# Kernel optimization log

Measured on AMD Instinct MI355X. Metric: run time of the kernel, lower is better.

The kernel has to match this reference:

```python
import jax, jax.numpy as jnp
import numpy as np

FP8_E4M3_MAX = 448.0  # matches the 448.0 constant in the torch module


def setup_inputs() -> dict:
    key = jax.random.key(0)
    kx, kw, kb = jax.random.split(key, 3)
    B, S, D_IN, D_OUT = 4, 2048, 4096, 4096
    x = jax.random.normal(kx, (B, S, D_IN), dtype=jnp.float32)
    # Simulate the __init__-time FP8 quantization of the linear weight.
    w = jax.random.normal(kw, (D_OUT, D_IN), dtype=jnp.float32) * 0.02
    amax = jnp.max(jnp.abs(w))
    weight_scale = FP8_E4M3_MAX / (amax + 1e-12)
    weight_fp8 = (w * weight_scale).astype(jnp.float8_e4m3fn)  # stored FP8 buffer
    weight_inv_scale = (1.0 / weight_scale).astype(jnp.float32)
    bias = jax.random.normal(kb, (D_OUT,), dtype=jnp.float32) * 0.02
    return {"x": x, "weight_fp8": weight_fp8,
            "weight_inv_scale": weight_inv_scale, "bias": bias}


def reference(x, weight_fp8, weight_inv_scale, bias):
    # forward: dequantize FP8 weight to compute dtype, scale, then dense linear
    w = weight_fp8.astype(x.dtype) * weight_inv_scale.astype(x.dtype)  # [D_OUT, D_IN]
    # F.linear(x, w, bias) == x @ w.T + bias
    return jnp.einsum('bsd,od->bso', x, w) + bias.astype(x.dtype)
```

## Files before the change

kernel.cpp:

```cpp
#include <hip/hip_runtime.h>
#include <hip/hip_bf16.h>
#include <stdint.h>
#include <stddef.h>

typedef __bf16 bf16x8 __attribute__((ext_vector_type(8)));
typedef float  f32x4  __attribute__((ext_vector_type(4)));

__device__ __forceinline__ float fp8e4m3_to_f32(uint32_t b) {
    uint32_t e = (b >> 3) & 15u, m = b & 7u;
    float mag;
    if (e == 0)
        mag = (float)m * (1.0f / 512.0f);
    else
        mag = __uint_as_float(((e + 120u) << 23) | (m << 20));
    return (b & 0x80u) ? -mag : mag;
}

__device__ __forceinline__ unsigned short f32_to_bf16_bits(float f) {
    uint32_t x = __float_as_uint(f);
    uint32_t r = x + 0x7fffu + ((x >> 16) & 1u);
    return (unsigned short)(r >> 16);
}

__device__ __forceinline__ void gload_lds16(const void* g, void* l) {
    __builtin_amdgcn_global_load_lds(
        (const __attribute__((address_space(1))) uint32_t*)g,
        (__attribute__((address_space(3))) uint32_t*)l,
        16, 0, 0);
}

__global__ void detect_kernel(const uint32_t* __restrict__ w,
                              uint32_t* __restrict__ flag) {
    __shared__ int sF, sB;
    if (threadIdx.x == 0) { sF = 1; sB = 1; }
    __syncthreads();
    int f32ok = 1, bf16ok = 1;
    #pragma unroll
    for (int i = 0; i < 16; ++i) {
        uint32_t u = w[threadIdx.x * 16 + i];
        if (u & 0x000FFFFFu) f32ok = 0;
        if (u & 0x000F000Fu) bf16ok = 0;
    }
    if (!f32ok)  atomicExch(&sF, 0);
    if (!bf16ok) atomicExch(&sB, 0);
    __syncthreads();
    if (threadIdx.x == 0)
        *flag = sF ? 0u : (sB ? 1u : 2u);
}

__global__ void cvt_x_kernel(const float* __restrict__ x,
                             unsigned short* __restrict__ out, size_t n8) {
    size_t stride = (size_t)gridDim.x * blockDim.x;
    for (size_t i = (size_t)blockIdx.x * blockDim.x + threadIdx.x; i < n8; i += stride) {
        const float4* p = (const float4*)(x + i * 8);
        float4 a = p[0], b = p[1];
        union { uint4 v; unsigned short s[8]; } o;
        o.s[0] = f32_to_bf16_bits(a.x); o.s[1] = f32_to_bf16_bits(a.y);
        o.s[2] = f32_to_bf16_bits(a.z); o.s[3] = f32_to_bf16_bits(a.w);
        o.s[4] = f32_to_bf16_bits(b.x); o.s[5] = f32_to_bf16_bits(b.y);
        o.s[6] = f32_to_bf16_bits(b.z); o.s[7] = f32_to_bf16_bits(b.w);
        *(uint4*)(out + i * 8) = o.v;
    }
}

__global__ void prep_w_kernel(const void* __restrict__ wsrc,
                              const uint32_t* __restrict__ flag,
                              unsigned short* __restrict__ out, size_t n8) {
    const uint32_t mode = *flag;
    size_t stride = (size_t)gridDim.x * blockDim.x;
    for (size_t i = (size_t)blockIdx.x * blockDim.x + threadIdx.x; i < n8; i += stride) {
        union { uint4 v; unsigned short s[8]; } o;
        if (mode == 0) {
            const float4* p = (const float4*)((const float*)wsrc + i * 8);
            float4 a = p[0], b = p[1];
            o.s[0] = f32_to_bf16_bits(a.x); o.s[1] = f32_to_bf16_bits(a.y);
            o.s[2] = f32_to_bf16_bits(a.z); o.s[3] = f32_to_bf16_bits(a.w);
            o.s[4] = f32_to_bf16_bits(b.x); o.s[5] = f32_to_bf16_bits(b.y);
            o.s[6] = f32_to_bf16_bits(b.z); o.s[7] = f32_to_bf16_bits(b.w);
        } else if (mode == 1) {
            o.v = *(const uint4*)((const unsigned short*)wsrc + i * 8);
        } else {
            union { uint2 v; uint8_t b[8]; } u;
            u.v = *(const uint2*)((const uint8_t*)wsrc + i * 8);
            #pragma unroll
            for (int j = 0; j < 8; ++j)
                o.s[j] = f32_to_bf16_bits(fp8e4m3_to_f32(u.b[j]));
        }
        *(uint4*)(out + i * 8) = o.v;
    }
}


#define GBM 256
#define GBN 256
#define GBK 64

#define LDA_(qm) do {                                                          \
    _Pragma("unroll") for (int m = 0; m < 4; ++m) {                            \
        Af[m][0] = *(const bf16x8*)(a0 + ((qm)*8192 + m*2048));                \
        Af[m][1] = *(const bf16x8*)(a1 + ((qm)*8192 + m*2048));                \
    }                                                                          \
} while (0)

#define LDB_(qn, Bf) do {                                                      \
    _Pragma("unroll") for (int n = 0; n < 2; ++n) {                            \
        Bf[n][0] = *(const bf16x8*)(b0 + ((qn)*4096 + n*2048));                \
        Bf[n][1] = *(const bf16x8*)(b1 + ((qn)*4096 + n*2048));                \
    }                                                                          \
} while (0)

#define MFMA_(qm, qn, Bf) do {                                                 \
    _Pragma("unroll") for (int m = 0; m < 4; ++m)                              \
    _Pragma("unroll") for (int n = 0; n < 2; ++n)                              \
    _Pragma("unroll") for (int ks = 0; ks < 2; ++ks)                           \
        acc[(qm)*4+m][(qn)*2+n] = __builtin_amdgcn_mfma_f32_16x16x32_bf16(     \
            Af[m][ks], Bf[n][ks], acc[(qm)*4+m][(qn)*2+n], 0, 0, 0);           \
} while (0)

#define STAGE_(gsrc, koff, ldst) do {                                          \
    const uint8_t* _p = (gsrc) + (koff);                                       \
    _Pragma("unroll") for (int j = 0; j < 4; ++j)                              \
        gload_lds16(_p + (size_t)j * 64 * KB2, (ldst) + (sdst + j*8192));      \
} while (0)

__global__ __launch_bounds__(512, 2)
void gemm256_fr(const unsigned short* __restrict__ A,
                const unsigned short* __restrict__ Bw,
                const float* __restrict__ invp,
                const float* __restrict__ bias,
                float* __restrict__ C, int M, int N, int K) {
    __shared__ unsigned short lds[2][2][GBM * GBK];
    char* ldsb = (char*)&lds[0][0][0];

    const size_t KB2 = (size_t)K * 2;
    const int KT = K / GBK;

    const int nwg = gridDim.x;
    const int b   = blockIdx.x;
    const int wg  = (b & 7) * (nwg >> 3) + (b >> 3);
    const int MT  = M / GBM;
    const int tm  = wg % MT;
    const int tn  = wg / MT;

    const int t     = threadIdx.x;
    const int lane  = t & 63;
    const int wid   = t >> 6;
    const int wm    = wid >> 2;
    const int wn    = wid & 3;
    const int laneQ = lane & 15;
    const int laneH = lane >> 4;
    const int xorv  = (laneQ & 7) << 4;
    const int lrow  = lane >> 3;
    const int lcb   = (lane & 7) ^ lrow;

    const int col0  = (0   + laneH * 16) ^ xorv;
    const int col1  = (64  + laneH * 16) ^ xorv;
    const int aoff0 = wm * 16384 + laneQ * 128 + col0;
    const int aoff1 = wm * 16384 + laneQ * 128 + col1;
    const int boff0 = wn * 8192  + laneQ * 128 + col0;
    const int boff1 = wn * 8192  + laneQ * 128 + col1;
    const int sdst  = wid * 1024 + lane * 16;

    const uint8_t* gA = (const uint8_t*)A +
        ((size_t)tm * GBM + wid * 8 + lrow) * KB2 + (size_t)lcb * 16;
    const uint8_t* gB = (const uint8_t*)Bw +
        ((size_t)tn * GBN + wid * 8 + lrow) * KB2 + (size_t)lcb * 16;

    f32x4 acc[8][4] = {};
    bf16x8 Af[4][2], B0[2][2], B1[2][2];

    STAGE_(gB, (size_t)0,   ldsb + 32768);
    STAGE_(gA, (size_t)0,   ldsb);
    STAGE_(gB, (size_t)128, ldsb + 65536 + 32768);
    STAGE_(gA, (size_t)128, ldsb + 65536);
    asm volatile("s_waitcnt vmcnt(8)" ::: "memory");
    __builtin_amdgcn_s_barrier();

    for (int kt = 0; kt < KT; ++kt) {
        const int coff = (kt & 1) << 16;
        const char* ldsA = ldsb + coff;
        const char* ldsB = ldsb + coff + 32768;
        const char* a0 = ldsA + aoff0;
        const char* a1 = ldsA + aoff1;
        const char* b0 = ldsB + boff0;
        const char* b1 = ldsB + boff1;
        char* ldsAw = (char*)ldsA;
        char* ldsBw = (char*)ldsB;
        const bool more = (kt + 2) < KT;
        const size_t kb2 = (size_t)(kt + 2) * 128;

        LDA_(0);
        LDB_(0, B0);
        __builtin_amdgcn_s_setprio(1);
        MFMA_(0, 0, B0);
        __builtin_amdgcn_s_setprio(0);
        LDB_(1, B1);
        __builtin_amdgcn_s_setprio(1);
        MFMA_(0, 1, B1);
        __builtin_amdgcn_s_setprio(0);
        LDA_(1);
        asm volatile("s_waitcnt lgkmcnt(0)" ::: "memory");
        __builtin_amdgcn_s_barrier();

        if (more) {
            STAGE_(gB, kb2, ldsBw);
            STAGE_(gA, kb2, ldsAw);
        }
        __builtin_amdgcn_s_setprio(1);
        MFMA_(1, 1, B1);
        MFMA_(1, 0, B0);
        __builtin_amdgcn_s_setprio(0);
        if (more) asm volatile("s_waitcnt vmcnt(8)" ::: "memory");
        else      asm volatile("s_waitcnt vmcnt(0)" ::: "memory");
        __builtin_amdgcn_s_barrier();
    }

    const float inv = *invp;
    float bv[4];
    #pragma unroll
    for (int n = 0; n < 4; ++n)
        bv[n] = bias[tn * GBN + wn * 64 + n * 16 + laneQ];

    #pragma unroll
    for (int m = 0; m < 8; ++m) {
        int rowb = tm * GBM + wm * 128 + m * 16 + laneH * 4;
        #pragma unroll
        for (int j = 0; j < 4; ++j) {
            float* cp = C + (size_t)(rowb + j) * N + tn * GBN + wn * 64;
            #pragma unroll
            for (int n = 0; n < 4; ++n)
                cp[n * 16 + laneQ] = acc[m][n][j] * inv + bv[n];
        }
    }
}

__global__ void naive_kernel(const float* __restrict__ x,
                             const void* __restrict__ wsrc,
                             const uint32_t* flag,
                             const float* __restrict__ invp,
                             const float* __restrict__ bias,
                             float* __restrict__ out, int M, int N, int K) {
    const uint32_t mode = flag ? *flag : 0u;
    size_t idx = (size_t)blockIdx.x * blockDim.x + threadIdx.x;
    if (idx >= (size_t)M * N) return;
    int m = (int)(idx / N), n = (int)(idx % N);
    const float* xr = x + (size_t)m * K;
    float s = 0.f;
    if (mode == 0) {
        const float* wr = (const float*)wsrc + (size_t)n * K;
        for (int k = 0; k < K; ++k) s += xr[k] * wr[k];
    } else if (mode == 1) {
        const unsigned short* wr = (const unsigned short*)wsrc + (size_t)n * K;
        for (int k = 0; k < K; ++k)
            s += xr[k] * __uint_as_float(((uint32_t)wr[k]) << 16);
    } else {
        const uint8_t* wr = (const uint8_t*)wsrc + (size_t)n * K;
        for (int k = 0; k < K; ++k) s += xr[k] * fp8e4m3_to_f32(wr[k]);
    }
    out[idx] = s * (*invp) + bias[n];
}

extern "C" void kernel_launch(void* const* d_in, const int* in_sizes, int n_in,
                              void* d_out, int out_size, void* d_ws, size_t ws_size,
                              hipStream_t stream) {
    const float*    x    = (const float*)d_in[0];
    const void*     wsrc = d_in[1];
    const float*    inv  = (const float*)d_in[2];
    const float*    bias = (const float*)d_in[3];
    float*          out  = (float*)d_out;

    const int K = in_sizes[1] / in_sizes[3];
    const int N = in_sizes[3];
    const int M = in_sizes[0] / K;

    const size_t needA = (size_t)M * K * sizeof(unsigned short);
    const size_t needB = (size_t)N * K * sizeof(unsigned short);

    const bool shape_ok = (M % GBM) == 0 && (N % GBN) == 0 && (K % GBK) == 0 &&
                          (K / GBK) >= 2 &&
                          (((M / GBM) * (N / GBN)) % 8) == 0;

    if (ws_size < needA + needB + 256 || !shape_ok) {
        size_t total = (size_t)M * N;
        uint32_t* flag = (ws_size >= 256) ? (uint32_t*)d_ws : nullptr;
        if (flag) detect_kernel<<<1, 256, 0, stream>>>((const uint32_t*)wsrc, flag);
        naive_kernel<<<(unsigned)((total + 255) / 256), 256, 0, stream>>>(
            x, wsrc, flag, inv, bias, out, M, N, K);
        return;
    }

    uint32_t*       flag = (uint32_t*)d_ws;
    unsigned short* Abf  = (unsigned short*)((char*)d_ws + 256);
    unsigned short* Wbf  = (unsigned short*)((char*)d_ws + 256 + needA);

    detect_kernel<<<1, 256, 0, stream>>>((const uint32_t*)wsrc, flag);
    cvt_x_kernel<<<2048, 256, 0, stream>>>(x, Abf, (size_t)M * K / 8);
    prep_w_kernel<<<2048, 256, 0, stream>>>(wsrc, flag, Wbf, (size_t)N * K / 8);

    dim3 grid((M / GBM) * (N / GBN));
    gemm256_fr<<<grid, 512, 0, stream>>>(Abf, Wbf, inv, bias, out, M, N, K);
}
```

Baseline: 297.4 us.

## Prefetch next tile's B fragments from LDS across the barrier

Restructures the main loop so the first B fragment set for the next k-tile is loaded from the other LDS buffer right after the end-of-iteration barrier, before the last MFMA group runs. The MFMA groups are reordered so that MFMA(1,0) runs before the barrier and MFMA(1,1) runs after it. This is meant to hide LDS read latency behind MFMA work and put more compute between the global-stage issue and the wait. In exchange it keeps an extra fragment set live across iterations, which raises register pressure, and it moves the global staging issue later relative to compute.

After: 301.5 us. Within noise of the previous version (+1.4%).

```diff
diff --git a/kernel.cpp b/kernel.cpp
--- a/kernel.cpp
+++ b/kernel.cpp
@@ -97,24 +97,26 @@
 
 #define LDA_(qm) do {                                                          \
     _Pragma("unroll") for (int m = 0; m < 4; ++m) {                            \
-        Af[m][0] = *(const bf16x8*)(a0 + ((qm)*8192 + m*2048));                \
-        Af[m][1] = *(const bf16x8*)(a1 + ((qm)*8192 + m*2048));                \
+        AF[m][0] = *(const bf16x8*)(ldsA + aoff0 + ((qm)*8192 + m*2048));      \
+        AF[m][1] = *(const bf16x8*)(ldsA + aoff1 + ((qm)*8192 + m*2048));      \
     }                                                                          \
 } while (0)
 
-#define LDB_(qn, Bf) do {                                                      \
+#define LDB_(base, qn, Bf) do {                                                \
     _Pragma("unroll") for (int n = 0; n < 2; ++n) {                            \
-        Bf[n][0] = *(const bf16x8*)(b0 + ((qn)*4096 + n*2048));                \
-        Bf[n][1] = *(const bf16x8*)(b1 + ((qn)*4096 + n*2048));                \
+        Bf[n][0] = *(const bf16x8*)((base) + boff0 + ((qn)*4096 + n*2048));    \
+        Bf[n][1] = *(const bf16x8*)((base) + boff1 + ((qn)*4096 + n*2048));    \
     }                                                                          \
 } while (0)
 
 #define MFMA_(qm, qn, Bf) do {                                                 \
+    __builtin_amdgcn_s_setprio(1);                                             \
     _Pragma("unroll") for (int m = 0; m < 4; ++m)                              \
     _Pragma("unroll") for (int n = 0; n < 2; ++n)                              \
     _Pragma("unroll") for (int ks = 0; ks < 2; ++ks)                           \
         acc[(qm)*4+m][(qn)*2+n] = __builtin_amdgcn_mfma_f32_16x16x32_bf16(     \
-            Af[m][ks], Bf[n][ks], acc[(qm)*4+m][(qn)*2+n], 0, 0, 0);           \
+            AF[m][ks], Bf[n][ks], acc[(qm)*4+m][(qn)*2+n], 0, 0, 0);           \
+    __builtin_amdgcn_s_setprio(0);                                             \
 } while (0)
 
 #define STAGE_(gsrc, koff, ldst) do {                                          \
@@ -124,7 +126,7 @@
 } while (0)
 
 __global__ __launch_bounds__(512, 2)
-void gemm256_fr(const unsigned short* __restrict__ A,
+void gemm256_pf(const unsigned short* __restrict__ A,
                 const unsigned short* __restrict__ Bw,
                 const float* __restrict__ invp,
                 const float* __restrict__ bias,
@@ -167,7 +169,7 @@
         ((size_t)tn * GBN + wid * 8 + lrow) * KB2 + (size_t)lcb * 16;
 
     f32x4 acc[8][4] = {};
-    bf16x8 Af[4][2], B0[2][2], B1[2][2];
+    bf16x8 AF[4][2], BX[2][2], BY[2][2];
 
     STAGE_(gB, (size_t)0,   ldsb + 32768);
     STAGE_(gA, (size_t)0,   ldsb);
@@ -175,30 +177,25 @@
     STAGE_(gA, (size_t)128, ldsb + 65536);
     asm volatile("s_waitcnt vmcnt(8)" ::: "memory");
     __builtin_amdgcn_s_barrier();
+    LDB_(ldsb + 32768, 0, BX);
 
     for (int kt = 0; kt < KT; ++kt) {
         const int coff = (kt & 1) << 16;
-        const char* ldsA = ldsb + coff;
-        const char* ldsB = ldsb + coff + 32768;
-        const char* a0 = ldsA + aoff0;
-        const char* a1 = ldsA + aoff1;
-        const char* b0 = ldsB + boff0;
-        const char* b1 = ldsB + boff1;
+        const char* ldsA  = ldsb + coff;
+        const char* ldsB  = ldsb + coff + 32768;
+        const char* ldsBn = ldsb + (coff ^ 65536) + 32768;
         char* ldsAw = (char*)ldsA;
         char* ldsBw = (char*)ldsB;
         const bool more = (kt + 2) < KT;
         const size_t kb2 = (size_t)(kt + 2) * 128;
 
         LDA_(0);
-        LDB_(0, B0);
-        __builtin_amdgcn_s_setprio(1);
-        MFMA_(0, 0, B0);
-        __builtin_amdgcn_s_setprio(0);
-        LDB_(1, B1);
-        __builtin_amdgcn_s_setprio(1);
-        MFMA_(0, 1, B1);
-        __builtin_amdgcn_s_setprio(0);
+        MFMA_(0, 0, BX);
+        LDB_(ldsB, 1, BY);
+        MFMA_(0, 1, BY);
         LDA_(1);
+        MFMA_(1, 0, BX);
+
         asm volatile("s_waitcnt lgkmcnt(0)" ::: "memory");
         __builtin_amdgcn_s_barrier();
 
@@ -206,13 +203,12 @@
             STAGE_(gB, kb2, ldsBw);
             STAGE_(gA, kb2, ldsAw);
         }
-        __builtin_amdgcn_s_setprio(1);
-        MFMA_(1, 1, B1);
-        MFMA_(1, 0, B0);
-        __builtin_amdgcn_s_setprio(0);
         if (more) asm volatile("s_waitcnt vmcnt(8)" ::: "memory");
         else      asm volatile("s_waitcnt vmcnt(0)" ::: "memory");
         __builtin_amdgcn_s_barrier();
+
+        if (kt + 1 < KT) LDB_(ldsBn, 0, BX);
+        MFMA_(1, 1, BY);
     }
 
     const float inv = *invp;
@@ -298,5 +294,5 @@
     prep_w_kernel<<<2048, 256, 0, stream>>>(wsrc, flag, Wbf, (size_t)N * K / 8);
 
     dim3 grid((M / GBM) * (N / GBN));
-    gemm256_fr<<<grid, 512, 0, stream>>>(Abf, Wbf, inv, bias, out, M, N, K);
-}
+    gemm256_pf<<<grid, 512, 0, stream>>>(Abf, Wbf, inv, bias, out, M, N, K);
+}
```
